# Kernel tuning notes

Measured on AMD Instinct MI355X. Metric: run time of the kernel, lower is better.

Reference implementation:

```python
import jax, jax.numpy as jnp
import numpy as np

N = 50000      # nodes
E = 800000     # edges (before self loops)
G = 64         # graphs in batch
F_IN = 11
HID = 64
C = 8
NEG_SLOPE = 0.2


def setup_inputs() -> dict:
    key = jax.random.key(0)
    ks = jax.random.split(key, 20)
    inp = {
        "x": jax.random.normal(ks[0], (N, F_IN), dtype=jnp.float32),
        "edge_index": jax.random.randint(ks[1], (2, E), 0, N, dtype=jnp.int64),
        "edge_attr": jax.random.normal(ks[2], (E, 17), dtype=jnp.float32),
        "batch": jnp.sort(jax.random.randint(ks[3], (N,), 0, G, dtype=jnp.int64)),
    }
    def glorot(k, shape):
        fan_in, fan_out = shape[0], shape[-1]
        s = jnp.sqrt(6.0 / (fan_in + fan_out))
        return jax.random.uniform(k, shape, jnp.float32, -s, s)
    # GATConv layers (heads=1): W [in,out], att vectors a_src/a_dst [out], bias [out]
    inp["W1"] = glorot(ks[4], (F_IN, HID)); inp["a1s"] = glorot(ks[5], (HID,)); inp["a1d"] = glorot(ks[6], (HID,)); inp["b1"] = jnp.zeros((HID,), jnp.float32)
    inp["W2"] = glorot(ks[7], (HID, HID)); inp["a2s"] = glorot(ks[8], (HID,)); inp["a2d"] = glorot(ks[9], (HID,)); inp["b2"] = jnp.zeros((HID,), jnp.float32)
    inp["W3"] = glorot(ks[10], (HID, C)); inp["a3s"] = glorot(ks[11], (C,)); inp["a3d"] = glorot(ks[12], (C,)); inp["b3"] = jnp.zeros((C,), jnp.float32)
    return inp


def _gat_layer(x, src, dst, W, a_s, a_d, b):
    # x: [N,in] -> h: [N,out]; single head, concat irrelevant for heads=1
    h = x @ W
    alpha_src = h @ a_s            # [N]
    alpha_dst = h @ a_d            # [N]
    e = jax.nn.leaky_relu(alpha_src[src] + alpha_dst[dst], negative_slope=NEG_SLOPE)  # [E']
    # segment-wise (per destination node) softmax over incoming edges
    m = jax.ops.segment_max(e, dst, num_segments=N)
    ex = jnp.exp(e - m[dst])
    denom = jax.ops.segment_sum(ex, dst, num_segments=N)
    alpha = ex / denom[dst]
    out = jax.ops.segment_sum(alpha[:, None] * h[src], dst, num_segments=N)
    return out + b


def reference(x, edge_index, edge_attr, batch, W1, a1s, a1d, b1, W2, a2s, a2d, b2, W3, a3s, a3d, b3):
    del edge_attr  # GATConv without edge_dim ignores edge_attr
    loop = jnp.arange(N, dtype=edge_index.dtype)
    src = jnp.concatenate([edge_index[0], loop])  # add self loops
    dst = jnp.concatenate([edge_index[1], loop])
    h = jax.nn.relu(_gat_layer(x, src, dst, W1, a1s, a1d, b1))
    h = jax.nn.relu(_gat_layer(h, src, dst, W2, a2s, a2d, b2))
    h = jax.nn.relu(_gat_layer(h, src, dst, W3, a3s, a3d, b3))
    # global mean pool over graphs
    counts = jax.ops.segment_sum(jnp.ones((N,), h.dtype), batch, num_segments=G)
    pooled = jax.ops.segment_sum(h, batch, num_segments=G) / jnp.maximum(counts, 1.0)[:, None]
    # dropout is identity in eval mode
    return jax.nn.sigmoid(pooled)
```

## Files before the change

### kernel.cpp

```cpp
#include <hip/hip_runtime.h>
#include <hip/hip_bf16.h>

#define NN 50000
#define EE 800000
#define GG 64
#define CC 8

#define NBKT 196
#define CHUNK 4096
#define NCHK 196
#define CAP 8192

__device__ __forceinline__ float lrelu(float z) { return fmaxf(z, 0.2f * z); }

__device__ __forceinline__ unsigned short f2bf(float v) {
    unsigned u = __float_as_uint(v);
    return (unsigned short)((u + 0x7FFFu + ((u >> 16) & 1u)) >> 16);
}
__device__ __forceinline__ float bf2f(unsigned short b) {
    return __uint_as_float(((unsigned)b) << 16);
}


__global__ __launch_bounds__(256) void kA1(const int* __restrict__ dst, int* __restrict__ G) {
    __shared__ int hist[NBKT];
    int t = threadIdx.x;
    for (int i = t; i < NBKT; i += 256) hist[i] = 0;
    __syncthreads();
    int e0 = blockIdx.x * CHUNK;
    int e1 = min(e0 + CHUNK, EE);
    for (int e = e0 + t; e < e1; e += 256) atomicAdd(&hist[dst[e] >> 8], 1);
    __syncthreads();
    for (int i = t; i < NBKT; i += 256) G[blockIdx.x * NBKT + i] = hist[i];
}

__global__ __launch_bounds__(256) void kA2(const int* __restrict__ G, int* __restrict__ offs,
                                           int* __restrict__ bT) {
    __shared__ int s[256];
    int t = threadIdx.x, j = blockIdx.x;
    int v = (t < NCHK) ? G[t * NBKT + j] : 0;
    s[t] = v;
    __syncthreads();
#pragma unroll
    for (int off = 1; off < 256; off <<= 1) {
        int u = (t >= off) ? s[t - off] : 0;
        __syncthreads();
        s[t] += u;
        __syncthreads();
    }
    if (t < NCHK) offs[t * NBKT + j] = s[t] - v;
    if (t == 255) bT[j] = s[255];
}

__global__ __launch_bounds__(256) void kA2b(const int* __restrict__ bT, int* __restrict__ bstart,
                                            float* __restrict__ pool, float* __restrict__ cntf,
                                            int* __restrict__ rowptr) {
    __shared__ int s[256];
    int t = threadIdx.x;
    int v = (t < NBKT) ? bT[t] : 0;
    s[t] = v;
    __syncthreads();
#pragma unroll
    for (int off = 1; off < 256; off <<= 1) {
        int u = (t >= off) ? s[t - off] : 0;
        __syncthreads();
        s[t] += u;
        __syncthreads();
    }
    if (t < NBKT) bstart[t] = s[t] - v;
    if (t == 0) { bstart[NBKT] = EE; rowptr[NN] = EE; }
    for (int i = t; i < GG * CC; i += 256) pool[i] = 0.f;
    if (t < GG) cntf[t] = 0.f;
}

__global__ __launch_bounds__(256) void kA3(const int* __restrict__ src, const int* __restrict__ dst,
                                           const int* __restrict__ offs, const int* __restrict__ bstart,
                                           unsigned* __restrict__ pairs) {
    __shared__ int cur[NBKT];
    int t = threadIdx.x, c = blockIdx.x;
    for (int i = t; i < NBKT; i += 256) cur[i] = bstart[i] + offs[c * NBKT + i];
    __syncthreads();
    int e0 = c * CHUNK, e1 = min(e0 + CHUNK, EE);
    for (int e = e0 + t; e < e1; e += 256) {
        int d = dst[e];
        int pos = atomicAdd(&cur[d >> 8], 1);
        pairs[pos] = (unsigned)src[e] | ((unsigned)(d & 255) << 16);
    }
}

__global__ __launch_bounds__(256) void kB(const unsigned* __restrict__ pairs, const int* __restrict__ bstart,
                                          int* __restrict__ col, int* __restrict__ rowptr) {
    __shared__ unsigned pL[CAP];
    __shared__ int hist[256];
    __shared__ int sc[256];
    int t = threadIdx.x, j = blockIdx.x;
    int start = bstart[j], end = bstart[j + 1];
    int cnt = end - start;
    if (cnt > CAP) cnt = CAP;
    int nb = j * 256;
    int nodeCnt = min(256, NN - nb);
    hist[t] = 0;
    __syncthreads();
    for (int i = t; i < cnt; i += 256) {
        unsigned p = pairs[start + i];
        pL[i] = p;
        atomicAdd(&hist[p >> 16], 1);
    }
    __syncthreads();
    int c = hist[t];
    sc[t] = c;
    __syncthreads();
#pragma unroll
    for (int off = 1; off < 256; off <<= 1) {
        int u = (t >= off) ? sc[t - off] : 0;
        __syncthreads();
        sc[t] += u;
        __syncthreads();
    }
    int excl = sc[t] - c;
    if (t < nodeCnt) rowptr[nb + t] = start + excl;
    hist[t] = excl;
    __syncthreads();
    for (int i = t; i < cnt; i += 256) {
        unsigned p = pL[i];
        int pos = atomicAdd(&hist[p >> 16], 1);
        col[start + pos] = (int)(p & 0xFFFFu);
    }
}


template <int IN>
__global__ __launch_bounds__(256) void k_mm64t(const float* __restrict__ x, const float* __restrict__ W,
                                               const float* __restrict__ avs, const float* __restrict__ avd,
                                               unsigned short* __restrict__ h, float* __restrict__ as_,
                                               float* __restrict__ ad_) {
    __shared__ float xT[IN * 68];
    __shared__ float Wl[IN * 64];
    __shared__ float avl[64], adl[64];
    int t = threadIdx.x;
    int nbase = blockIdx.x * 64;
    for (int idx = t; idx < IN * 64; idx += 256) Wl[idx] = W[idx];
    if (t < 64) { avl[t] = avs[t]; adl[t] = avd[t]; }
    for (int idx = t; idx < 64 * IN; idx += 256) {
        int n = idx / IN, k = idx - n * IN;
        int gn = nbase + n;
        if (gn >= NN) gn = NN - 1;
        xT[k * 68 + n] = x[gn * IN + k];
    }
    __syncthreads();
    int f0 = (t & 15) * 4;
    int n0 = (t >> 4) * 4;
    float a00=0,a01=0,a02=0,a03=0, a10=0,a11=0,a12=0,a13=0;
    float a20=0,a21=0,a22=0,a23=0, a30=0,a31=0,a32=0,a33=0;
#pragma unroll 4
    for (int k = 0; k < IN; k++) {
        float4 xv = *(const float4*)&xT[k * 68 + n0];
        float4 wv = *(const float4*)&Wl[k * 64 + f0];
        a00 += xv.x * wv.x; a01 += xv.x * wv.y; a02 += xv.x * wv.z; a03 += xv.x * wv.w;
        a10 += xv.y * wv.x; a11 += xv.y * wv.y; a12 += xv.y * wv.z; a13 += xv.y * wv.w;
        a20 += xv.z * wv.x; a21 += xv.z * wv.y; a22 += xv.z * wv.z; a23 += xv.z * wv.w;
        a30 += xv.w * wv.x; a31 += xv.w * wv.y; a32 += xv.w * wv.z; a33 += xv.w * wv.w;
    }
    float4 av = *(const float4*)&avl[f0];
    float4 dv = *(const float4*)&adl[f0];
    float vs[4], vd[4];
    vs[0] = a00*av.x + a01*av.y + a02*av.z + a03*av.w;
    vs[1] = a10*av.x + a11*av.y + a12*av.z + a13*av.w;
    vs[2] = a20*av.x + a21*av.y + a22*av.z + a23*av.w;
    vs[3] = a30*av.x + a31*av.y + a32*av.z + a33*av.w;
    vd[0] = a00*dv.x + a01*dv.y + a02*dv.z + a03*dv.w;
    vd[1] = a10*dv.x + a11*dv.y + a12*dv.z + a13*dv.w;
    vd[2] = a20*dv.x + a21*dv.y + a22*dv.z + a23*dv.w;
    vd[3] = a30*dv.x + a31*dv.y + a32*dv.z + a33*dv.w;
#pragma unroll
    for (int o = 1; o < 16; o <<= 1) {
#pragma unroll
        for (int ni = 0; ni < 4; ni++) {
            vs[ni] += __shfl_xor(vs[ni], o);
            vd[ni] += __shfl_xor(vd[ni], o);
        }
    }
    ushort4* h4 = (ushort4*)h;
    int nn0 = nbase + n0;
    float rows[4][4] = {{a00,a01,a02,a03},{a10,a11,a12,a13},{a20,a21,a22,a23},{a30,a31,a32,a33}};
#pragma unroll
    for (int ni = 0; ni < 4; ni++) {
        if (nn0 + ni < NN) {
            ushort4 pv;
            pv.x = f2bf(rows[ni][0]); pv.y = f2bf(rows[ni][1]);
            pv.z = f2bf(rows[ni][2]); pv.w = f2bf(rows[ni][3]);
            h4[(nn0 + ni) * 16 + (t & 15)] = pv;
            if ((t & 15) == 0) { as_[nn0 + ni] = vs[ni]; ad_[nn0 + ni] = vd[ni]; }
        }
    }
}

__global__ __launch_bounds__(256) void k_mm8(const float* __restrict__ x, const float* __restrict__ W,
                                             const float* __restrict__ avs, const float* __restrict__ avd,
                                             unsigned short* __restrict__ h3, float* __restrict__ as_,
                                             float* __restrict__ ad_) {
    __shared__ float Wl[512];
    for (int idx = threadIdx.x; idx < 512; idx += 256) Wl[idx] = W[idx];
    __syncthreads();
    int node = blockIdx.x * 4 + (threadIdx.x >> 6);
    int lane = threadIdx.x & 63;
    if (node >= NN) return;
    int f = lane & 7, kc = lane >> 3;
    float xv = x[node * 64 + lane];
    float acc = 0.f;
#pragma unroll
    for (int j = 0; j < 8; j++) {
        int k = kc * 8 + j;
        acc += __shfl(xv, k) * Wl[k * 8 + f];
    }
    acc += __shfl_xor(acc, 8);
    acc += __shfl_xor(acc, 16);
    acc += __shfl_xor(acc, 32);
    if (lane < 8) h3[node * 8 + lane] = f2bf(acc);
    float vs = 0.f, vd = 0.f;
    if (lane < 8) {
        vs = acc * avs[lane];
        vd = acc * avd[lane];
    }
    vs += __shfl_xor(vs, 1); vs += __shfl_xor(vs, 2); vs += __shfl_xor(vs, 4);
    vd += __shfl_xor(vd, 1); vd += __shfl_xor(vd, 2); vd += __shfl_xor(vd, 4);
    if (lane == 0) {
        as_[node] = vs;
        ad_[node] = vd;
    }
}


__global__ __launch_bounds__(256) void k_agg64(const unsigned short* __restrict__ h,
                                               const int* __restrict__ rowptr,
                                               const int* __restrict__ col, const float* __restrict__ as_,
                                               const float* __restrict__ ad_, const float* __restrict__ bias,
                                               float* __restrict__ out) {
    __shared__ uint2 ws[4][64];
    int wid = threadIdx.x >> 6;
    int node = blockIdx.x * 4 + wid;
    int lane = threadIdx.x & 63;
    int rp0 = rowptr[node];
    int deg = rowptr[node + 1] - rp0;
    float adn = ad_[node];
    float zself = lrelu(as_[node] + adn);
    const ushort4* hb = (const ushort4*)h;
    int f = lane & 15, eg = lane >> 4;
    float4 acc = make_float4(0.f, 0.f, 0.f, 0.f);
    if (deg <= 64) {
        int s = 0;
        float z = -1e30f;
        if (lane < deg) {
            s = col[rp0 + lane];
            z = lrelu(as_[s] + adn);
        }
        float M = z;
#pragma unroll
        for (int o = 32; o; o >>= 1) M = fmaxf(M, __shfl_xor(M, o));
        M = fmaxf(M, zself);
        float ex = (lane < deg) ? __expf(z - M) : 0.f;
        float exs = __expf(zself - M);
        float sum = ex;
#pragma unroll
        for (int o = 32; o; o >>= 1) sum += __shfl_xor(sum, o);
        float inv = 1.f / (sum + exs);
        float wl = ex * inv;
        ws[wid][lane] = make_uint2(__float_as_uint(wl), (unsigned)s);
        __syncthreads();
        const uint4* wsp = (const uint4*)&ws[wid][0];
        for (int base = 0; base < deg; base += 8) {
            uint4 p = wsp[(base >> 1) + eg];
            float wa = __uint_as_float(p.x);
            float wb = __uint_as_float(p.z);
            ushort4 ha = hb[p.y * 16 + f];
            ushort4 hc = hb[p.w * 16 + f];
            acc.x += wa * bf2f(ha.x) + wb * bf2f(hc.x);
            acc.y += wa * bf2f(ha.y) + wb * bf2f(hc.y);
            acc.z += wa * bf2f(ha.z) + wb * bf2f(hc.z);
            acc.w += wa * bf2f(ha.w) + wb * bf2f(hc.w);
        }
        if (eg == 0) {
            float w0 = exs * inv;
            ushort4 hv = hb[node * 16 + f];
            acc.x += w0 * bf2f(hv.x);
            acc.y += w0 * bf2f(hv.y);
            acc.z += w0 * bf2f(hv.z);
            acc.w += w0 * bf2f(hv.w);
        }
    } else {
        __syncthreads();
        float m = -1e30f, l = 0.f;
        for (int i = lane; i < deg; i += 64) {
            float z = lrelu(as_[col[rp0 + i]] + adn);
            float mn = fmaxf(m, z);
            l = l * __expf(m - mn) + __expf(z - mn);
            m = mn;
        }
        if (lane == 0) {
            float mn = fmaxf(m, zself);
            l = l * __expf(m - mn) + __expf(zself - mn);
            m = mn;
        }
#pragma unroll
        for (int o = 32; o; o >>= 1) {
            float mo = __shfl_xor(m, o), lo = __shfl_xor(l, o);
            float mn = fmaxf(m, mo);
            l = l * __expf(m - mn) + lo * __expf(mo - mn);
            m = mn;
        }
        float Em = m;
        float inv = 1.f / l;
        for (int base = 0; base < deg; base += 4) {
            int i = base + eg;
            if (i < deg) {
                int sv = col[rp0 + i];
                float al = __expf(lrelu(as_[sv] + adn) - Em) * inv;
                ushort4 hv = hb[sv * 16 + f];
                acc.x += al * bf2f(hv.x);
                acc.y += al * bf2f(hv.y);
                acc.z += al * bf2f(hv.z);
                acc.w += al * bf2f(hv.w);
            }
        }
        if (eg == 0) {
            float al = __expf(zself - Em) * inv;
            ushort4 hv = hb[node * 16 + f];
            acc.x += al * bf2f(hv.x);
            acc.y += al * bf2f(hv.y);
            acc.z += al * bf2f(hv.z);
            acc.w += al * bf2f(hv.w);
        }
    }
#pragma unroll
    for (int o = 16; o <= 32; o <<= 1) {
        acc.x += __shfl_xor(acc.x, o);
        acc.y += __shfl_xor(acc.y, o);
        acc.z += __shfl_xor(acc.z, o);
        acc.w += __shfl_xor(acc.w, o);
    }
    if (eg == 0) {
        float4 bv = ((const float4*)bias)[f];
        float4 o4;
        o4.x = fmaxf(acc.x + bv.x, 0.f);
        o4.y = fmaxf(acc.y + bv.y, 0.f);
        o4.z = fmaxf(acc.z + bv.z, 0.f);
        o4.w = fmaxf(acc.w + bv.w, 0.f);
        ((float4*)out)[node * 16 + f] = o4;
    }
}

__global__ __launch_bounds__(256) void k_agg8(const unsigned short* __restrict__ h,
                                              const int* __restrict__ rowptr,
                                              const int* __restrict__ col, const float* __restrict__ as_,
                                              const float* __restrict__ ad_, const float* __restrict__ bias,
                                              float* __restrict__ out) {
    __shared__ uint2 ws[4][64];
    int wid = threadIdx.x >> 6;
    int node = blockIdx.x * 4 + wid;
    int lane = threadIdx.x & 63;
    int rp0 = rowptr[node];
    int deg = rowptr[node + 1] - rp0;
    float adn = ad_[node];
    float zself = lrelu(as_[node] + adn);
    const ushort2* h2v = (const ushort2*)h;
    int f = lane & 3, eg = lane >> 2;
    float2 acc = make_float2(0.f, 0.f);
    if (deg <= 64) {
        int s = 0;
        float z = -1e30f;
        if (lane < deg) {
            s = col[rp0 + lane];
            z = lrelu(as_[s] + adn);
        }
        float M = z;
#pragma unroll
        for (int o = 32; o; o >>= 1) M = fmaxf(M, __shfl_xor(M, o));
        M = fmaxf(M, zself);
        float ex = (lane < deg) ? __expf(z - M) : 0.f;
        float exs = __expf(zself - M);
        float sum = ex;
#pragma unroll
        for (int o = 32; o; o >>= 1) sum += __shfl_xor(sum, o);
        float inv = 1.f / (sum + exs);
        float wl = ex * inv;
        ws[wid][lane] = make_uint2(__float_as_uint(wl), (unsigned)s);
        __syncthreads();
        const uint4* wsp = (const uint4*)&ws[wid][0];
        for (int base = 0; base < deg; base += 32) {
            uint4 p = wsp[(base >> 1) + eg];
            float wa = __uint_as_float(p.x);
            float wb = __uint_as_float(p.z);
            ushort2 ha = h2v[p.y * 4 + f];
            ushort2 hc = h2v[p.w * 4 + f];
            acc.x += wa * bf2f(ha.x) + wb * bf2f(hc.x);
            acc.y += wa * bf2f(ha.y) + wb * bf2f(hc.y);
        }
        if (eg == 0) {
            float w0 = exs * inv;
            ushort2 hv = h2v[node * 4 + f];
            acc.x += w0 * bf2f(hv.x);
            acc.y += w0 * bf2f(hv.y);
        }
    } else {
        __syncthreads();
        float m = -1e30f, l = 0.f;
        for (int i = lane; i < deg; i += 64) {
            float z = lrelu(as_[col[rp0 + i]] + adn);
            float mn = fmaxf(m, z);
            l = l * __expf(m - mn) + __expf(z - mn);
            m = mn;
        }
        if (lane == 0) {
            float mn = fmaxf(m, zself);
            l = l * __expf(m - mn) + __expf(zself - mn);
            m = mn;
        }
#pragma unroll
        for (int o = 32; o; o >>= 1) {
            float mo = __shfl_xor(m, o), lo = __shfl_xor(l, o);
            float mn = fmaxf(m, mo);
            l = l * __expf(m - mn) + lo * __expf(mo - mn);
            m = mn;
        }
        float Em = m;
        float inv = 1.f / l;
        for (int base = 0; base < deg; base += 16) {
            int i = base + eg;
            if (i < deg) {
                int sv = col[rp0 + i];
                float al = __expf(lrelu(as_[sv] + adn) - Em) * inv;
                ushort2 hv = h2v[sv * 4 + f];
                acc.x += al * bf2f(hv.x);
                acc.y += al * bf2f(hv.y);
            }
        }
        if (eg == 0) {
            float al = __expf(zself - Em) * inv;
            ushort2 hv = h2v[node * 4 + f];
            acc.x += al * bf2f(hv.x);
            acc.y += al * bf2f(hv.y);
        }
    }
#pragma unroll
    for (int o = 4; o <= 32; o <<= 1) {
        acc.x += __shfl_xor(acc.x, o);
        acc.y += __shfl_xor(acc.y, o);
    }
    if (eg == 0) {
        float2 bv = ((const float2*)bias)[f];
        float2 o2;
        o2.x = fmaxf(acc.x + bv.x, 0.f);
        o2.y = fmaxf(acc.y + bv.y, 0.f);
        ((float2*)out)[node * 4 + f] = o2;
    }
}


__global__ __launch_bounds__(256) void k_pool(const float* __restrict__ h3, const int* __restrict__ batch,
                                              float* __restrict__ pool, float* __restrict__ cntf) {
    __shared__ float pl[GG * CC + GG];
    for (int idx = threadIdx.x; idx < GG * CC + GG; idx += 256) pl[idx] = 0.f;
    __syncthreads();
    int node = blockIdx.x * 256 + threadIdx.x;
    if (node < NN) {
        int g = batch[node];
#pragma unroll
        for (int c = 0; c < CC; c++) atomicAdd(&pl[g * CC + c], h3[node * CC + c]);
        atomicAdd(&pl[GG * CC + g], 1.0f);
    }
    __syncthreads();
    for (int idx = threadIdx.x; idx < GG * CC + GG; idx += 256) {
        float v = pl[idx];
        if (idx < GG * CC)
            atomicAdd(&pool[idx], v);
        else
            atomicAdd(&cntf[idx - GG * CC], v);
    }
}

__global__ void k_final(const float* __restrict__ pool, const float* __restrict__ cntf,
                        float* __restrict__ out) {
    int t = threadIdx.x;
    if (t < GG * CC) {
        int g = t >> 3;
        float c = fmaxf(cntf[g], 1.0f);
        float v = pool[t] / c;
        out[t] = 1.0f / (1.0f + __expf(-v));
    }
}


extern "C" void kernel_launch(void* const* d_in, const int* in_sizes, int n_in,
                              void* d_out, int out_size, void* d_ws, size_t ws_size,
                              hipStream_t stream) {
    const float* x   = (const float*)d_in[0];
    const int*   ei  = (const int*)d_in[1];
    const int*   bat = (const int*)d_in[3];
    const float* W1  = (const float*)d_in[4];
    const float* a1s = (const float*)d_in[5];
    const float* a1d = (const float*)d_in[6];
    const float* b1  = (const float*)d_in[7];
    const float* W2  = (const float*)d_in[8];
    const float* a2s = (const float*)d_in[9];
    const float* a2d = (const float*)d_in[10];
    const float* b2  = (const float*)d_in[11];
    const float* W3  = (const float*)d_in[12];
    const float* a3s = (const float*)d_in[13];
    const float* a3d = (const float*)d_in[14];
    const float* b3  = (const float*)d_in[15];
    float* out = (float*)d_out;

    float* hA  = (float*)d_ws;
    float* hB  = hA + NN * 64;
    float* h3a = hB + NN * 64;
    float* h3b = h3a + NN * 8;
    float* as_ = h3b + NN * 8;
    float* ad_ = as_ + NN;
    int* rowptr  = (int*)(ad_ + NN);
    int* col     = rowptr + NN + 1;
    int* G       = col + EE;
    int* offs    = G + NCHK * NBKT;
    int* bT      = offs + NCHK * NBKT;
    int* bstart  = bT + NBKT;
    float* pool  = (float*)(bstart + NBKT + 1);
    float* cntf  = pool + GG * CC;
    unsigned* pairs = (unsigned*)hA;

    unsigned short* hA16 = (unsigned short*)hA;
    unsigned short* h316 = (unsigned short*)h3a;

    const int NB4  = (NN + 3) / 4;
    const int NB64 = (NN + 63) / 64;
    const int NBN  = (NN + 255) / 256;

    const int* srcE = ei;
    const int* dstE = ei + EE;

    kA1<<<NCHK, 256, 0, stream>>>(dstE, G);
    kA2<<<NBKT, 256, 0, stream>>>(G, offs, bT);
    kA2b<<<1, 256, 0, stream>>>(bT, bstart, pool, cntf, rowptr);
    kA3<<<NCHK, 256, 0, stream>>>(srcE, dstE, offs, bstart, pairs);
    kB<<<NBKT, 256, 0, stream>>>(pairs, bstart, col, rowptr);

    k_mm64t<11><<<NB64, 256, 0, stream>>>(x, W1, a1s, a1d, hA16, as_, ad_);
    k_agg64<<<NB4, 256, 0, stream>>>(hA16, rowptr, col, as_, ad_, b1, hB);
    k_mm64t<64><<<NB64, 256, 0, stream>>>(hB, W2, a2s, a2d, hA16, as_, ad_);
    k_agg64<<<NB4, 256, 0, stream>>>(hA16, rowptr, col, as_, ad_, b2, hB);
    k_mm8<<<NB4, 256, 0, stream>>>(hB, W3, a3s, a3d, h316, as_, ad_);
    k_agg8<<<NB4, 256, 0, stream>>>(h316, rowptr, col, as_, ad_, b3, h3b);
    k_pool<<<NBN, 256, 0, stream>>>(h3b, bat, pool, cntf);
    k_final<<<1, 512, 0, stream>>>(pool, cntf, out);
}
```

Baseline: 283.6 us.

## Fuse CSR build stages with layer-1 matmul and pooling to cut launches

Merges the dst histogram into the first-layer 11→64 matmul kernel, using 782 chunks of 1024 edges so the chunk count matches the matmul grid. The bucket-start scan is folded into the per-bucket scan, and the partition and sort kernels each recompute it redundantly. Pool and final sigmoid become one kernel that uses a last-block atomic counter. The point is to cut kernel launches and the serial tiny-kernel gaps, at the cost of redundant scans per block and a longer per-bucket scan over 782 chunks. The workspace layout is reorganised so pairs no longer alias the hA buffer, which the fused matmul now writes at the same time.

```diff
diff --git a/kernel.cpp b/kernel.cpp
--- a/kernel.cpp
+++ b/kernel.cpp
@@ -1,5 +1,4 @@
 #include <hip/hip_runtime.h>
-#include <hip/hip_bf16.h>
 
 #define NN 50000
 #define EE 800000
@@ -7,12 +6,13 @@
 #define CC 8
 
 #define NBKT 196
-#define CHUNK 4096
-#define NCHK 196
+#define NCHK 782
+#define CHUNK 1024
 #define CAP 8192
 
+__device__ unsigned g_done = 0;
+
 __device__ __forceinline__ float lrelu(float z) { return fmaxf(z, 0.2f * z); }
-
 __device__ __forceinline__ unsigned short f2bf(float v) {
     unsigned u = __float_as_uint(v);
     return (unsigned short)((u + 0x7FFFu + ((u >> 16) & 1u)) >> 16);
@@ -22,138 +22,33 @@
 }
 
 
-__global__ __launch_bounds__(256) void kA1(const int* __restrict__ dst, int* __restrict__ G) {
+__global__ __launch_bounds__(256) void k0_mm11_hist(const float* __restrict__ x, const float* __restrict__ W,
+                                                    const float* __restrict__ avs, const float* __restrict__ avd,
+                                                    unsigned short* __restrict__ h, float* __restrict__ as_,
+                                                    float* __restrict__ ad_, const int* __restrict__ dst,
+                                                    int* __restrict__ G) {
+    __shared__ float xT[11 * 68];
+    __shared__ float Wl[11 * 64];
+    __shared__ float avl[64], adl[64];
     __shared__ int hist[NBKT];
     int t = threadIdx.x;
-    for (int i = t; i < NBKT; i += 256) hist[i] = 0;
-    __syncthreads();
-    int e0 = blockIdx.x * CHUNK;
-    int e1 = min(e0 + CHUNK, EE);
-    for (int e = e0 + t; e < e1; e += 256) atomicAdd(&hist[dst[e] >> 8], 1);
-    __syncthreads();
-    for (int i = t; i < NBKT; i += 256) G[blockIdx.x * NBKT + i] = hist[i];
-}
-
-__global__ __launch_bounds__(256) void kA2(const int* __restrict__ G, int* __restrict__ offs,
-                                           int* __restrict__ bT) {
-    __shared__ int s[256];
-    int t = threadIdx.x, j = blockIdx.x;
-    int v = (t < NCHK) ? G[t * NBKT + j] : 0;
-    s[t] = v;
-    __syncthreads();
-#pragma unroll
-    for (int off = 1; off < 256; off <<= 1) {
-        int u = (t >= off) ? s[t - off] : 0;
-        __syncthreads();
-        s[t] += u;
-        __syncthreads();
-    }
-    if (t < NCHK) offs[t * NBKT + j] = s[t] - v;
-    if (t == 255) bT[j] = s[255];
-}
-
-__global__ __launch_bounds__(256) void kA2b(const int* __restrict__ bT, int* __restrict__ bstart,
-                                            float* __restrict__ pool, float* __restrict__ cntf,
-                                            int* __restrict__ rowptr) {
-    __shared__ int s[256];
-    int t = threadIdx.x;
-    int v = (t < NBKT) ? bT[t] : 0;
-    s[t] = v;
-    __syncthreads();
-#pragma unroll
-    for (int off = 1; off < 256; off <<= 1) {
-        int u = (t >= off) ? s[t - off] : 0;
-        __syncthreads();
-        s[t] += u;
-        __syncthreads();
-    }
-    if (t < NBKT) bstart[t] = s[t] - v;
-    if (t == 0) { bstart[NBKT] = EE; rowptr[NN] = EE; }
-    for (int i = t; i < GG * CC; i += 256) pool[i] = 0.f;
-    if (t < GG) cntf[t] = 0.f;
-}
-
-__global__ __launch_bounds__(256) void kA3(const int* __restrict__ src, const int* __restrict__ dst,
-                                           const int* __restrict__ offs, const int* __restrict__ bstart,
-                                           unsigned* __restrict__ pairs) {
-    __shared__ int cur[NBKT];
-    int t = threadIdx.x, c = blockIdx.x;
-    for (int i = t; i < NBKT; i += 256) cur[i] = bstart[i] + offs[c * NBKT + i];
-    __syncthreads();
-    int e0 = c * CHUNK, e1 = min(e0 + CHUNK, EE);
-    for (int e = e0 + t; e < e1; e += 256) {
-        int d = dst[e];
-        int pos = atomicAdd(&cur[d >> 8], 1);
-        pairs[pos] = (unsigned)src[e] | ((unsigned)(d & 255) << 16);
-    }
-}
-
-__global__ __launch_bounds__(256) void kB(const unsigned* __restrict__ pairs, const int* __restrict__ bstart,
-                                          int* __restrict__ col, int* __restrict__ rowptr) {
-    __shared__ unsigned pL[CAP];
-    __shared__ int hist[256];
-    __shared__ int sc[256];
-    int t = threadIdx.x, j = blockIdx.x;
-    int start = bstart[j], end = bstart[j + 1];
-    int cnt = end - start;
-    if (cnt > CAP) cnt = CAP;
-    int nb = j * 256;
-    int nodeCnt = min(256, NN - nb);
-    hist[t] = 0;
-    __syncthreads();
-    for (int i = t; i < cnt; i += 256) {
-        unsigned p = pairs[start + i];
-        pL[i] = p;
-        atomicAdd(&hist[p >> 16], 1);
-    }
-    __syncthreads();
-    int c = hist[t];
-    sc[t] = c;
-    __syncthreads();
-#pragma unroll
-    for (int off = 1; off < 256; off <<= 1) {
-        int u = (t >= off) ? sc[t - off] : 0;
-        __syncthreads();
-        sc[t] += u;
-        __syncthreads();
-    }
-    int excl = sc[t] - c;
-    if (t < nodeCnt) rowptr[nb + t] = start + excl;
-    hist[t] = excl;
-    __syncthreads();
-    for (int i = t; i < cnt; i += 256) {
-        unsigned p = pL[i];
-        int pos = atomicAdd(&hist[p >> 16], 1);
-        col[start + pos] = (int)(p & 0xFFFFu);
-    }
-}
-
-
-template <int IN>
-__global__ __launch_bounds__(256) void k_mm64t(const float* __restrict__ x, const float* __restrict__ W,
-                                               const float* __restrict__ avs, const float* __restrict__ avd,
-                                               unsigned short* __restrict__ h, float* __restrict__ as_,
-                                               float* __restrict__ ad_) {
-    __shared__ float xT[IN * 68];
-    __shared__ float Wl[IN * 64];
-    __shared__ float avl[64], adl[64];
-    int t = threadIdx.x;
     int nbase = blockIdx.x * 64;
-    for (int idx = t; idx < IN * 64; idx += 256) Wl[idx] = W[idx];
+    for (int idx = t; idx < 11 * 64; idx += 256) Wl[idx] = W[idx];
     if (t < 64) { avl[t] = avs[t]; adl[t] = avd[t]; }
-    for (int idx = t; idx < 64 * IN; idx += 256) {
-        int n = idx / IN, k = idx - n * IN;
+    for (int idx = t; idx < 64 * 11; idx += 256) {
+        int n = idx / 11, k = idx - n * 11;
         int gn = nbase + n;
         if (gn >= NN) gn = NN - 1;
-        xT[k * 68 + n] = x[gn * IN + k];
-    }
+        xT[k * 68 + n] = x[gn * 11 + k];
+    }
+    for (int i = t; i < NBKT; i += 256) hist[i] = 0;
     __syncthreads();
     int f0 = (t & 15) * 4;
     int n0 = (t >> 4) * 4;
     float a00=0,a01=0,a02=0,a03=0, a10=0,a11=0,a12=0,a13=0;
     float a20=0,a21=0,a22=0,a23=0, a30=0,a31=0,a32=0,a33=0;
-#pragma unroll 4
-    for (int k = 0; k < IN; k++) {
+#pragma unroll
+    for (int k = 0; k < 11; k++) {
         float4 xv = *(const float4*)&xT[k * 68 + n0];
         float4 wv = *(const float4*)&Wl[k * 64 + f0];
         a00 += xv.x * wv.x; a01 += xv.x * wv.y; a02 += xv.x * wv.z; a03 += xv.x * wv.w;
@@ -193,7 +88,197 @@
             if ((t & 15) == 0) { as_[nn0 + ni] = vs[ni]; ad_[nn0 + ni] = vd[ni]; }
         }
     }
-}
+    int e0 = blockIdx.x * CHUNK;
+    int e1 = min(e0 + CHUNK, EE);
+    for (int e = e0 + t; e < e1; e += 256) atomicAdd(&hist[dst[e] >> 8], 1);
+    __syncthreads();
+    for (int i = t; i < NBKT; i += 256) G[blockIdx.x * NBKT + i] = hist[i];
+}
+
+
+__global__ __launch_bounds__(256) void k1_scan(const int* __restrict__ G, int* __restrict__ offs,
+                                               int* __restrict__ bT, float* __restrict__ pool,
+                                               float* __restrict__ cntf, int* __restrict__ rowptr) {
+    __shared__ int s[256];
+    int t = threadIdx.x, j = blockIdx.x;
+    int c0 = t * 4;
+    int v0 = (c0 + 0 < NCHK) ? G[(c0 + 0) * NBKT + j] : 0;
+    int v1 = (c0 + 1 < NCHK) ? G[(c0 + 1) * NBKT + j] : 0;
+    int v2 = (c0 + 2 < NCHK) ? G[(c0 + 2) * NBKT + j] : 0;
+    int v3 = (c0 + 3 < NCHK) ? G[(c0 + 3) * NBKT + j] : 0;
+    int tsum = v0 + v1 + v2 + v3;
+    s[t] = tsum;
+    __syncthreads();
+#pragma unroll
+    for (int off = 1; off < 256; off <<= 1) {
+        int u = (t >= off) ? s[t - off] : 0;
+        __syncthreads();
+        s[t] += u;
+        __syncthreads();
+    }
+    int excl = s[t] - tsum;
+    if (c0 + 0 < NCHK) offs[(c0 + 0) * NBKT + j] = excl;
+    if (c0 + 1 < NCHK) offs[(c0 + 1) * NBKT + j] = excl + v0;
+    if (c0 + 2 < NCHK) offs[(c0 + 2) * NBKT + j] = excl + v0 + v1;
+    if (c0 + 3 < NCHK) offs[(c0 + 3) * NBKT + j] = excl + v0 + v1 + v2;
+    if (t == 255) bT[j] = s[255];
+    if (j == 0) {
+        for (int i = t; i < GG * CC; i += 256) pool[i] = 0.f;
+        if (t < GG) cntf[t] = 0.f;
+        if (t == 0) rowptr[NN] = EE;
+    }
+}
+
+
+__global__ __launch_bounds__(256) void k2_part(const int* __restrict__ src, const int* __restrict__ dst,
+                                               const int* __restrict__ offs, const int* __restrict__ bT,
+                                               unsigned* __restrict__ pairs) {
+    __shared__ int s[256];
+    __shared__ int bst[NBKT];
+    __shared__ int cur[NBKT];
+    int t = threadIdx.x, c = blockIdx.x;
+    int v = (t < NBKT) ? bT[t] : 0;
+    s[t] = v;
+    __syncthreads();
+#pragma unroll
+    for (int off = 1; off < 256; off <<= 1) {
+        int u = (t >= off) ? s[t - off] : 0;
+        __syncthreads();
+        s[t] += u;
+        __syncthreads();
+    }
+    if (t < NBKT) bst[t] = s[t] - v;
+    __syncthreads();
+    for (int i = t; i < NBKT; i += 256) cur[i] = bst[i] + offs[c * NBKT + i];
+    __syncthreads();
+    int e0 = c * CHUNK, e1 = min(e0 + CHUNK, EE);
+    for (int e = e0 + t; e < e1; e += 256) {
+        int d = dst[e];
+        int pos = atomicAdd(&cur[d >> 8], 1);
+        pairs[pos] = (unsigned)src[e] | ((unsigned)(d & 255) << 16);
+    }
+}
+
+
+__global__ __launch_bounds__(256) void k3_sort(const unsigned* __restrict__ pairs, const int* __restrict__ bT,
+                                               int* __restrict__ col, int* __restrict__ rowptr) {
+    __shared__ unsigned pL[CAP];
+    __shared__ int hist[256];
+    __shared__ int sc[256];
+    int t = threadIdx.x, j = blockIdx.x;
+    int v = (t < NBKT) ? bT[t] : 0;
+    hist[t] = v;
+    __syncthreads();
+#pragma unroll
+    for (int off = 1; off < 256; off <<= 1) {
+        int u = (t >= off) ? hist[t - off] : 0;
+        __syncthreads();
+        hist[t] += u;
+        __syncthreads();
+    }
+    if (t == j) { sc[0] = hist[t] - v; sc[1] = v; }
+    __syncthreads();
+    int start = sc[0];
+    int cnt = sc[1];
+    if (cnt > CAP) cnt = CAP;
+    int nb = j * 256;
+    int nodeCnt = min(256, NN - nb);
+    __syncthreads();
+    hist[t] = 0;
+    __syncthreads();
+    for (int i = t; i < cnt; i += 256) {
+        unsigned p = pairs[start + i];
+        pL[i] = p;
+        atomicAdd(&hist[p >> 16], 1);
+    }
+    __syncthreads();
+    int c2 = hist[t];
+    sc[t] = c2;
+    __syncthreads();
+#pragma unroll
+    for (int off = 1; off < 256; off <<= 1) {
+        int u = (t >= off) ? sc[t - off] : 0;
+        __syncthreads();
+        sc[t] += u;
+        __syncthreads();
+    }
+    int excl = sc[t] - c2;
+    if (t < nodeCnt) rowptr[nb + t] = start + excl;
+    hist[t] = excl;
+    __syncthreads();
+    for (int i = t; i < cnt; i += 256) {
+        unsigned p = pL[i];
+        int pos = atomicAdd(&hist[p >> 16], 1);
+        col[start + pos] = (int)(p & 0xFFFFu);
+    }
+}
+
+
+__global__ __launch_bounds__(256) void k_mm64t(const float* __restrict__ x, const float* __restrict__ W,
+                                               const float* __restrict__ avs, const float* __restrict__ avd,
+                                               unsigned short* __restrict__ h, float* __restrict__ as_,
+                                               float* __restrict__ ad_) {
+    __shared__ float xT[64 * 68];
+    __shared__ float Wl[64 * 64];
+    __shared__ float avl[64], adl[64];
+    int t = threadIdx.x;
+    int nbase = blockIdx.x * 64;
+    for (int idx = t; idx < 64 * 64; idx += 256) Wl[idx] = W[idx];
+    if (t < 64) { avl[t] = avs[t]; adl[t] = avd[t]; }
+    for (int idx = t; idx < 64 * 64; idx += 256) {
+        int n = idx / 64, k = idx - n * 64;
+        int gn = nbase + n;
+        if (gn >= NN) gn = NN - 1;
+        xT[k * 68 + n] = x[gn * 64 + k];
+    }
+    __syncthreads();
+    int f0 = (t & 15) * 4;
+    int n0 = (t >> 4) * 4;
+    float a00=0,a01=0,a02=0,a03=0, a10=0,a11=0,a12=0,a13=0;
+    float a20=0,a21=0,a22=0,a23=0, a30=0,a31=0,a32=0,a33=0;
+#pragma unroll 4
+    for (int k = 0; k < 64; k++) {
+        float4 xv = *(const float4*)&xT[k * 68 + n0];
+        float4 wv = *(const float4*)&Wl[k * 64 + f0];
+        a00 += xv.x * wv.x; a01 += xv.x * wv.y; a02 += xv.x * wv.z; a03 += xv.x * wv.w;
+        a10 += xv.y * wv.x; a11 += xv.y * wv.y; a12 += xv.y * wv.z; a13 += xv.y * wv.w;
+        a20 += xv.z * wv.x; a21 += xv.z * wv.y; a22 += xv.z * wv.z; a23 += xv.z * wv.w;
+        a30 += xv.w * wv.x; a31 += xv.w * wv.y; a32 += xv.w * wv.z; a33 += xv.w * wv.w;
+    }
+    float4 av = *(const float4*)&avl[f0];
+    float4 dv = *(const float4*)&adl[f0];
+    float vs[4], vd[4];
+    vs[0] = a00*av.x + a01*av.y + a02*av.z + a03*av.w;
+    vs[1] = a10*av.x + a11*av.y + a12*av.z + a13*av.w;
+    vs[2] = a20*av.x + a21*av.y + a22*av.z + a23*av.w;
+    vs[3] = a30*av.x + a31*av.y + a32*av.z + a33*av.w;
+    vd[0] = a00*dv.x + a01*dv.y + a02*dv.z + a03*dv.w;
+    vd[1] = a10*dv.x + a11*dv.y + a12*dv.z + a13*dv.w;
+    vd[2] = a20*dv.x + a21*dv.y + a22*dv.z + a23*dv.w;
+    vd[3] = a30*dv.x + a31*dv.y + a32*dv.z + a33*dv.w;
+#pragma unroll
+    for (int o = 1; o < 16; o <<= 1) {
+#pragma unroll
+        for (int ni = 0; ni < 4; ni++) {
+            vs[ni] += __shfl_xor(vs[ni], o);
+            vd[ni] += __shfl_xor(vd[ni], o);
+        }
+    }
+    ushort4* h4 = (ushort4*)h;
+    int nn0 = nbase + n0;
+    float rows[4][4] = {{a00,a01,a02,a03},{a10,a11,a12,a13},{a20,a21,a22,a23},{a30,a31,a32,a33}};
+#pragma unroll
+    for (int ni = 0; ni < 4; ni++) {
+        if (nn0 + ni < NN) {
+            ushort4 pv;
+            pv.x = f2bf(rows[ni][0]); pv.y = f2bf(rows[ni][1]);
+            pv.z = f2bf(rows[ni][2]); pv.w = f2bf(rows[ni][3]);
+            h4[(nn0 + ni) * 16 + (t & 15)] = pv;
+            if ((t & 15) == 0) { as_[nn0 + ni] = vs[ni]; ad_[nn0 + ni] = vd[ni]; }
+        }
+    }
+}
+
 
 __global__ __launch_bounds__(256) void k_mm8(const float* __restrict__ x, const float* __restrict__ W,
                                              const float* __restrict__ avs, const float* __restrict__ avd,
@@ -456,12 +541,15 @@
 }
 
 
-__global__ __launch_bounds__(256) void k_pool(const float* __restrict__ h3, const int* __restrict__ batch,
-                                              float* __restrict__ pool, float* __restrict__ cntf) {
+__global__ __launch_bounds__(256) void k9_poolfinal(const float* __restrict__ h3, const int* __restrict__ batch,
+                                                    float* __restrict__ pool, float* __restrict__ cntf,
+                                                    float* __restrict__ out) {
     __shared__ float pl[GG * CC + GG];
-    for (int idx = threadIdx.x; idx < GG * CC + GG; idx += 256) pl[idx] = 0.f;
-    __syncthreads();
-    int node = blockIdx.x * 256 + threadIdx.x;
+    __shared__ int lastFlag;
+    int t = threadIdx.x;
+    for (int idx = t; idx < GG * CC + GG; idx += 256) pl[idx] = 0.f;
+    __syncthreads();
+    int node = blockIdx.x * 256 + t;
     if (node < NN) {
         int g = batch[node];
 #pragma unroll
@@ -469,23 +557,31 @@
         atomicAdd(&pl[GG * CC + g], 1.0f);
     }
     __syncthreads();
-    for (int idx = threadIdx.x; idx < GG * CC + GG; idx += 256) {
+    for (int idx = t; idx < GG * CC + GG; idx += 256) {
         float v = pl[idx];
         if (idx < GG * CC)
             atomicAdd(&pool[idx], v);
         else
             atomicAdd(&cntf[idx - GG * CC], v);
     }
-}
-
-__global__ void k_final(const float* __restrict__ pool, const float* __restrict__ cntf,
-                        float* __restrict__ out) {
-    int t = threadIdx.x;
-    if (t < GG * CC) {
-        int g = t >> 3;
-        float c = fmaxf(cntf[g], 1.0f);
-        float v = pool[t] / c;
-        out[t] = 1.0f / (1.0f + __expf(-v));
+    __syncthreads();
+    if (t == 0) {
+        __threadfence();
+        unsigned r = __hip_atomic_fetch_add(&g_done, 1u, __ATOMIC_ACQ_REL, __HIP_MEMORY_SCOPE_AGENT);
+        lastFlag = (r == (unsigned)(NBKT - 1));
+    }
+    __syncthreads();
+    if (lastFlag) {
+        __threadfence();
+        for (int i = t; i < GG * CC; i += 256) {
+            int g = i >> 3;
+            float c = __hip_atomic_load(&cntf[g], __ATOMIC_RELAXED, __HIP_MEMORY_SCOPE_AGENT);
+            float p = __hip_atomic_load(&pool[i], __ATOMIC_RELAXED, __HIP_MEMORY_SCOPE_AGENT);
+            float v = p / fmaxf(c, 1.0f);
+            out[i] = 1.0f / (1.0f + __expf(-v));
+        }
+        if (t == 0)
+            __hip_atomic_store(&g_done, 0u, __ATOMIC_RELAXED, __HIP_MEMORY_SCOPE_AGENT);
     }
 }
 
@@ -510,44 +606,37 @@
     const float* b3  = (const float*)d_in[15];
     float* out = (float*)d_out;
 
-    float* hA  = (float*)d_ws;
-    float* hB  = hA + NN * 64;
-    float* h3a = hB + NN * 64;
-    float* h3b = h3a + NN * 8;
-    float* as_ = h3b + NN * 8;
-    float* ad_ = as_ + NN;
-    int* rowptr  = (int*)(ad_ + NN);
-    int* col     = rowptr + NN + 1;
-    int* G       = col + EE;
-    int* offs    = G + NCHK * NBKT;
-    int* bT      = offs + NCHK * NBKT;
-    int* bstart  = bT + NBKT;
-    float* pool  = (float*)(bstart + NBKT + 1);
-    float* cntf  = pool + GG * CC;
-    unsigned* pairs = (unsigned*)hA;
-
-    unsigned short* hA16 = (unsigned short*)hA;
-    unsigned short* h316 = (unsigned short*)h3a;
+    float* fb = (float*)d_ws;
+    unsigned short* hA16 = (unsigned short*)fb;
+    float* hB   = fb + NN * 32;
+    unsigned short* h316 = (unsigned short*)(hB + NN * 64);
+    float* h3b  = hB + NN * 64 + NN * 4;
+    float* as_  = h3b + NN * 8;
+    float* ad_  = as_ + NN;
+    int* rowptr = (int*)(ad_ + NN);
+    int* col    = rowptr + NN + 1;
+    int* G      = col + EE;
+    int* offs   = G + NCHK * NBKT;
+    int* bT     = offs + NCHK * NBKT;
+    unsigned* pairs = (unsigned*)(bT + 256);
+    float* pool = (float*)(pairs + EE);
+    float* cntf = pool + GG * CC;
 
     const int NB4  = (NN + 3) / 4;
     const int NB64 = (NN + 63) / 64;
-    const int NBN  = (NN + 255) / 256;
 
     const int* srcE = ei;
     const int* dstE = ei + EE;
 
-    kA1<<<NCHK, 256, 0, stream>>>(dstE, G);
-    kA2<<<NBKT, 256, 0, stream>>>(G, offs, bT);
-    kA2b<<<1, 256, 0, stream>>>(bT, bstart, pool, cntf, rowptr);
-    kA3<<<NCHK, 256, 0, stream>>>(srcE, dstE, offs, bstart, pairs);
-    kB<<<NBKT, 256, 0, stream>>>(pairs, bstart, col, rowptr);
-
-    k_mm64t<11><<<NB64, 256, 0, stream>>>(x, W1, a1s, a1d, hA16, as_, ad_);
+    k0_mm11_hist<<<NB64, 256, 0, stream>>>(x, W1, a1s, a1d, hA16, as_, ad_, dstE, G);
+    k1_scan<<<NBKT, 256, 0, stream>>>(G, offs, bT, pool, cntf, rowptr);
+    k2_part<<<NCHK, 256, 0, stream>>>(srcE, dstE, offs, bT, pairs);
+    k3_sort<<<NBKT, 256, 0, stream>>>(pairs, bT, col, rowptr);
+
     k_agg64<<<NB4, 256, 0, stream>>>(hA16, rowptr, col, as_, ad_, b1, hB);
-    k_mm64t<64><<<NB64, 256, 0, stream>>>(hB, W2, a2s, a2d, hA16, as_, ad_);
+    k_mm64t<<<NB64, 256, 0, stream>>>(hB, W2, a2s, a2d, hA16, as_, ad_);
     k_agg64<<<NB4, 256, 0, stream>>>(hA16, rowptr, col, as_, ad_, b2, hB);
     k_mm8<<<NB4, 256, 0, stream>>>(hB, W3, a3s, a3d, h316, as_, ad_);
     k_agg8<<<NB4, 256, 0, stream>>>(h316, rowptr, col, as_, ad_, b3, h3b);
-    k_pool<<<NBN, 256, 0, stream>>>(h3b, bat, pool, cntf);
-    k_final<<<1, 512, 0, stream>>>(pool, cntf, out);
-}
+    k9_poolfinal<<<NBKT, 256, 0, stream>>>(h3b, bat, pool, cntf, out);
+}
```

Result: faster. 276.6 us (-2.4%).
